# Performance work log

Measured on AMD Instinct MI355X. Metric: run time of the kernel, lower is better.

Reference implementation:

```python
import jax, jax.numpy as jnp
import numpy as np

TEMP = 0.05
EPS = 1e-8  # F.cosine_similarity eps

def setup_inputs() -> dict:
    key = jax.random.key(0)
    k1, k2 = jax.random.split(key)
    cls = jax.random.normal(k1, (4096, 1024), dtype=jnp.float32)
    hidden = jax.random.normal(k2, (4096, 1024), dtype=jnp.float32)
    return {"cls": cls, "hidden": hidden}

def _normalize(x):
    # matches F.cosine_similarity: divide by max(||x||, eps)
    n = jnp.sqrt(jnp.sum(x * x, axis=-1, keepdims=True))
    return x / jnp.maximum(n, EPS)

def reference(cls, hidden):
    a = _normalize(cls)          # [B, H]
    b = _normalize(hidden)       # [B, H]
    sim = jnp.einsum('ih,jh->ij', a, b) / TEMP  # [B, B] cosine sims / temp
    # cross-entropy with labels = arange(B): mean(logsumexp(row) - diag)
    lse = jax.nn.logsumexp(sim, axis=-1)        # [B]
    diag = jnp.diagonal(sim)                    # [B]
    return jnp.mean(lse - diag)
```

## Files before the change

### kernel.cpp

```cpp
#include <hip/hip_runtime.h>
#include <hip/hip_bf16.h>

typedef __attribute__((ext_vector_type(8))) short bf16x8;
typedef __attribute__((ext_vector_type(4))) float f32x4;

#define B_ROWS 4096
#define H_DIM  1024
#define TEMP_INV 20.0f
#define BM 256
#define BK 64
#define NT (H_DIM / BK)
#define NBN (B_ROWS / BM)

__device__ __forceinline__ void gload_lds16(const void* g, void* l) {
  __builtin_amdgcn_global_load_lds(
      (const __attribute__((address_space(1))) void*)g,
      (__attribute__((address_space(3))) void*)l, 16, 0, 0);
}

__global__ __launch_bounds__(256) void normalize_kernel(
    const float* __restrict__ cls, const float* __restrict__ hid,
    __hip_bfloat16* __restrict__ Abf, __hip_bfloat16* __restrict__ Bbf)
{
  const int w = threadIdx.x >> 6, lane = threadIdx.x & 63;
  const int r = blockIdx.x * 4 + w;
  const int rr = r & (B_ROWS - 1);
  const float* src = ((r < B_ROWS) ? cls : hid) + (size_t)rr * H_DIM;
  __hip_bfloat16* dst = ((r < B_ROWS) ? Abf : Bbf) + (size_t)rr * H_DIM;

  float4 v[4];
  float ss = 0.f;
  #pragma unroll
  for (int j = 0; j < 4; j++) {
    v[j] = reinterpret_cast<const float4*>(src)[j * 64 + lane];
    ss += v[j].x * v[j].x + v[j].y * v[j].y + v[j].z * v[j].z + v[j].w * v[j].w;
  }
  #pragma unroll
  for (int off = 1; off < 64; off <<= 1) ss += __shfl_xor(ss, off, 64);
  const float scale = 1.0f / fmaxf(sqrtf(ss), 1e-8f);

  #pragma unroll
  for (int j = 0; j < 4; j++) {
    union { ushort4 u; __hip_bfloat16 h[4]; } o;
    o.h[0] = __float2bfloat16(v[j].x * scale);
    o.h[1] = __float2bfloat16(v[j].y * scale);
    o.h[2] = __float2bfloat16(v[j].z * scale);
    o.h[3] = __float2bfloat16(v[j].w * scale);
    reinterpret_cast<ushort4*>(dst)[j * 64 + lane] = o.u;
  }
}


#define LDS_RD_A(BUF, MB)                                                     \
  { _Pragma("unroll") for (int mi = 0; mi < 4; mi++) {                        \
      _Pragma("unroll") for (int ks = 0; ks < 2; ks++) {                      \
        af[mi][ks] = *(const bf16x8*)(&As[BUF][(rA2 ^ (ks << 6)) + ((MB) + mi) * 2048]); } } }

#define LDS_RD_B(BUF, NB)                                                     \
  { _Pragma("unroll") for (int ni = 0; ni < 2; ni++) {                        \
      _Pragma("unroll") for (int ks = 0; ks < 2; ks++) {                      \
        bfr[(NB) + ni][ks] = *(const bf16x8*)(&Bs[BUF][(rB2 ^ (ks << 6)) + ((NB) + ni) * 2048]); } } }

#define MFMA16(MB, NB)                                                        \
  { __builtin_amdgcn_s_setprio(1);                                            \
    _Pragma("unroll") for (int mi = 0; mi < 4; mi++) {                        \
      _Pragma("unroll") for (int ni = 0; ni < 2; ni++) {                      \
        _Pragma("unroll") for (int ks = 0; ks < 2; ks++) {                    \
          acc[(MB) + mi][(NB) + ni] = __builtin_amdgcn_mfma_f32_16x16x32_bf16(\
              af[mi][ks], bfr[(NB) + ni][ks], acc[(MB) + mi][(NB) + ni], 0, 0, 0); } } } \
    __builtin_amdgcn_s_setprio(0); }

#define BARB() __builtin_amdgcn_s_barrier()

#define STAGE_A(BUF, TT, C)                                                   \
  gload_lds16(Abase + (size_t)(row0 + (C) * 64 + srow) * 2048 + (TT) * 128 + scolb, \
              &As[BUF][(C) * 8192 + tid * 16])
#define STAGE_B(BUF, TT, C)                                                   \
  gload_lds16(Bbase + (size_t)(col0 + (C) * 64 + srow) * 2048 + (TT) * 128 + scolb, \
              &Bs[BUF][(C) * 8192 + tid * 16])

#define KTILE(BUF, T_)                                                        \
  { const int Tn = (T_) + 1;                                                  \
    LDS_RD_A(BUF, 0);                                                         \
    if (Tn < NT) { STAGE_B(BUF ^ 1, Tn, 2); STAGE_B(BUF ^ 1, Tn, 3); }        \
    BARB(); MFMA16(0, 0); BARB();                                             \
    LDS_RD_B(BUF, 2);                                                         \
    if ((T_) + 2 < NT) { STAGE_A(BUF, (T_) + 2, 0); STAGE_A(BUF, (T_) + 2, 2); } \
    BARB(); MFMA16(0, 2); BARB();                                             \
    LDS_RD_A(BUF, 4);                                                         \
    if ((T_) + 2 < NT) { STAGE_B(BUF, (T_) + 2, 0); STAGE_B(BUF, (T_) + 2, 1); } \
    BARB(); MFMA16(4, 0); BARB();                                             \
    if ((T_) + 2 < NT) {                                                      \
      STAGE_A(BUF, (T_) + 2, 1); STAGE_A(BUF, (T_) + 2, 3);                   \
      asm volatile("s_waitcnt vmcnt(6)" ::: "memory");                        \
    } else if (Tn < NT) {                                                     \
      asm volatile("s_waitcnt vmcnt(0)" ::: "memory");                        \
    }                                                                         \
    BARB();                                                                   \
    if (Tn < NT) { LDS_RD_B(BUF ^ 1, 0); }                                    \
    MFMA16(4, 2); BARB(); }

__global__ __launch_bounds__(512, 2) void gemm_kernel(
    const __hip_bfloat16* __restrict__ A, const __hip_bfloat16* __restrict__ Bm,
    float* __restrict__ pp, float* __restrict__ diag)
{
  __shared__ __align__(16) char As[2][32768];
  __shared__ __align__(16) char Bs[2][32768];

  const int tid  = threadIdx.x;
  const int lane = tid & 63;
  const int w    = tid >> 6;
  const int wm   = w >> 2, wn = w & 3;

  const int fid = blockIdx.y * NBN + blockIdx.x;
  const int swz = (fid & 7) * 32 + (fid >> 3);
  const int bm = swz >> 4, bn = swz & 15;

  const long row0 = (long)bm * BM, col0 = (long)bn * BM;
  const char* Abase = (const char*)A;
  const char* Bbase = (const char*)Bm;

  const int srow  = tid >> 3;
  const int scolb = ((tid & 7) ^ ((tid >> 3) & 7)) << 4;

  const int dsw = (lane & 7) << 4;
  const int rA2 = (((wm * 128 + (lane & 15)) * 128) + ((lane >> 4) * 16)) ^ dsw;
  const int rB2 = (((wn * 64  + (lane & 15)) * 128) + ((lane >> 4) * 16)) ^ dsw;

  f32x4 acc[8][4] = {};
  bf16x8 af[4][2], bfr[4][2];

  #pragma unroll
  for (int c = 0; c < 4; c++) STAGE_A(0, 0, c);
  #pragma unroll
  for (int c = 0; c < 4; c++) STAGE_B(0, 0, c);
  STAGE_A(1, 1, 0); STAGE_A(1, 1, 2);
  STAGE_B(1, 1, 0); STAGE_B(1, 1, 1);
  STAGE_A(1, 1, 1); STAGE_A(1, 1, 3);
  asm volatile("s_waitcnt vmcnt(6)" ::: "memory");
  BARB();
  LDS_RD_B(0, 0);

  #pragma unroll 1
  for (int T = 0; T < NT; T += 2) {
    KTILE(0, T);
    KTILE(1, T + 1);
  }

  const bool isdiag = (bm == bn);
  const int g = lane >> 4;
  __syncthreads();
  float* lds_p = (float*)&As[0][0];

  #pragma unroll
  for (int m = 0; m < 8; m++) {
    const int rowb = (int)row0 + wm * 128 + m * 16 + g * 4;
    float p[4] = {0.f, 0.f, 0.f, 0.f};
    #pragma unroll
    for (int n = 0; n < 4; n++) {
      const int colb = (int)col0 + wn * 64 + n * 16 + (lane & 15);
      #pragma unroll
      for (int r = 0; r < 4; r++) {
        float sim = acc[m][n][r] * TEMP_INV;
        if (isdiag && (rowb + r == colb)) diag[rowb + r] = sim;
        p[r] += __expf(sim);
      }
    }
    #pragma unroll
    for (int r = 0; r < 4; r++) {
      float s = p[r];
      s += __shfl_xor(s, 1, 64);
      s += __shfl_xor(s, 2, 64);
      s += __shfl_xor(s, 4, 64);
      s += __shfl_xor(s, 8, 64);
      if ((lane & 15) == 0)
        lds_p[wn * 256 + wm * 128 + m * 16 + g * 4 + r] = s;
    }
  }
  __syncthreads();
  if (tid < 256) {
    float s = lds_p[tid] + lds_p[256 + tid] + lds_p[512 + tid] + lds_p[768 + tid];
    pp[(size_t)bn * B_ROWS + row0 + tid] = s;
  }
}

__global__ __launch_bounds__(1024) void finalize_kernel(
    const float* __restrict__ pp, const float* __restrict__ diag,
    float* __restrict__ out)
{
  int tid = threadIdx.x;
  float acc = 0.f;
  for (int i = tid; i < B_ROWS; i += 1024) {
    float s = 0.f;
    #pragma unroll
    for (int j = 0; j < NBN; j++) s += pp[(size_t)j * B_ROWS + i];
    acc += logf(s) - diag[i];
  }
  #pragma unroll
  for (int off = 1; off < 64; off <<= 1) acc += __shfl_xor(acc, off, 64);
  __shared__ float wsum[16];
  if ((tid & 63) == 0) wsum[tid >> 6] = acc;
  __syncthreads();
  if (tid == 0) {
    float t = 0.f;
    #pragma unroll
    for (int i = 0; i < 16; i++) t += wsum[i];
    out[0] = t * (1.0f / B_ROWS);
  }
}

extern "C" void kernel_launch(void* const* d_in, const int* in_sizes, int n_in,
                              void* d_out, int out_size, void* d_ws, size_t ws_size,
                              hipStream_t stream)
{
  const float* cls = (const float*)d_in[0];
  const float* hid = (const float*)d_in[1];
  float* out = (float*)d_out;
  char* ws = (char*)d_ws;

  __hip_bfloat16* Abf = (__hip_bfloat16*)ws;
  __hip_bfloat16* Bbf = (__hip_bfloat16*)(ws + (size_t)B_ROWS * H_DIM * 2);
  float* pp   = (float*)(ws + (size_t)B_ROWS * H_DIM * 4);
  float* diag = pp + (size_t)NBN * B_ROWS;

  hipLaunchKernelGGL(normalize_kernel, dim3(2 * B_ROWS / 4), dim3(256), 0, stream,
                     cls, hid, Abf, Bbf);
  hipLaunchKernelGGL(gemm_kernel, dim3(B_ROWS / BM, B_ROWS / BM), dim3(512), 0, stream,
                     Abf, Bbf, pp, diag);
  hipLaunchKernelGGL(finalize_kernel, dim3(1), dim3(1024), 0, stream,
                     pp, diag, out);
}
```

Baseline: 119.1 us.

## Restructure GEMM to 256x128 tiles, BK=32, triple-buffered LDS pipeline

Changes the fused cosine-sim GEMM from 256x256 tiles with 8 waves and a hand-interleaved double-buffered BK=64 schedule to 256x128 tiles with 4 waves, BK=32 and a three-stage LDS ring. Each iteration issues loads two tiles ahead, then reads fragments and runs 32 MFMAs. This aims for more blocks (512), a simpler schedule and deeper prefetch, with less LDS per block. The cost is less data reuse per block, more barriers and K iterations, and twice as many partial-sum rows for the finalize kernel. The finalize kernel loops over NBN, which is now 32.

```diff
diff --git a/kernel.cpp b/kernel.cpp
--- a/kernel.cpp
+++ b/kernel.cpp
@@ -8,9 +8,11 @@
 #define H_DIM  1024
 #define TEMP_INV 20.0f
 #define BM 256
-#define BK 64
+#define BN 128
+#define BK 32
 #define NT (H_DIM / BK)
-#define NBN (B_ROWS / BM)
+#define NBM (B_ROWS / BM)
+#define NBN (B_ROWS / BN)
 
 __device__ __forceinline__ void gload_lds16(const void* g, void* l) {
   __builtin_amdgcn_global_load_lds(
@@ -51,103 +53,88 @@
 }
 
 
-#define LDS_RD_A(BUF, MB)                                                     \
-  { _Pragma("unroll") for (int mi = 0; mi < 4; mi++) {                        \
-      _Pragma("unroll") for (int ks = 0; ks < 2; ks++) {                      \
-        af[mi][ks] = *(const bf16x8*)(&As[BUF][(rA2 ^ (ks << 6)) + ((MB) + mi) * 2048]); } } }
-
-#define LDS_RD_B(BUF, NB)                                                     \
-  { _Pragma("unroll") for (int ni = 0; ni < 2; ni++) {                        \
-      _Pragma("unroll") for (int ks = 0; ks < 2; ks++) {                      \
-        bfr[(NB) + ni][ks] = *(const bf16x8*)(&Bs[BUF][(rB2 ^ (ks << 6)) + ((NB) + ni) * 2048]); } } }
-
-#define MFMA16(MB, NB)                                                        \
+#define STAGE_A(BUF, TT, C)                                                   \
+  gload_lds16(Abase + (size_t)(row0 + (C) * 64 + srow) * 2048 + (TT) * 64 + scolb, \
+              &As[BUF][(C) * 4096 + tid * 16])
+#define STAGE_B(BUF, TT, C)                                                   \
+  gload_lds16(Bbase + (size_t)(col0 + (C) * 64 + srow) * 2048 + (TT) * 64 + scolb, \
+              &Bs[BUF][(C) * 4096 + tid * 16])
+
+#define STAGE6(BUF, TT)                                                       \
+  { STAGE_A(BUF, TT, 0); STAGE_A(BUF, TT, 1); STAGE_A(BUF, TT, 2);            \
+    STAGE_A(BUF, TT, 3); STAGE_B(BUF, TT, 0); STAGE_B(BUF, TT, 1); }
+
+#define RDFRAGS(BC)                                                           \
+  { _Pragma("unroll") for (int mi = 0; mi < 8; mi++)                          \
+      af[mi] = *(const bf16x8*)(&As[BC][rA + mi * 1024]);                     \
+    _Pragma("unroll") for (int ni = 0; ni < 4; ni++)                          \
+      bfr[ni] = *(const bf16x8*)(&Bs[BC][rB + ni * 1024]); }
+
+#define MFMA32()                                                              \
   { __builtin_amdgcn_s_setprio(1);                                            \
-    _Pragma("unroll") for (int mi = 0; mi < 4; mi++) {                        \
-      _Pragma("unroll") for (int ni = 0; ni < 2; ni++) {                      \
-        _Pragma("unroll") for (int ks = 0; ks < 2; ks++) {                    \
-          acc[(MB) + mi][(NB) + ni] = __builtin_amdgcn_mfma_f32_16x16x32_bf16(\
-              af[mi][ks], bfr[(NB) + ni][ks], acc[(MB) + mi][(NB) + ni], 0, 0, 0); } } } \
+    _Pragma("unroll") for (int mi = 0; mi < 8; mi++) {                        \
+      _Pragma("unroll") for (int ni = 0; ni < 4; ni++) {                      \
+        acc[mi][ni] = __builtin_amdgcn_mfma_f32_16x16x32_bf16(                \
+            af[mi], bfr[ni], acc[mi][ni], 0, 0, 0); } }                       \
     __builtin_amdgcn_s_setprio(0); }
 
 #define BARB() __builtin_amdgcn_s_barrier()
 
-#define STAGE_A(BUF, TT, C)                                                   \
-  gload_lds16(Abase + (size_t)(row0 + (C) * 64 + srow) * 2048 + (TT) * 128 + scolb, \
-              &As[BUF][(C) * 8192 + tid * 16])
-#define STAGE_B(BUF, TT, C)                                                   \
-  gload_lds16(Bbase + (size_t)(col0 + (C) * 64 + srow) * 2048 + (TT) * 128 + scolb, \
-              &Bs[BUF][(C) * 8192 + tid * 16])
-
-#define KTILE(BUF, T_)                                                        \
-  { const int Tn = (T_) + 1;                                                  \
-    LDS_RD_A(BUF, 0);                                                         \
-    if (Tn < NT) { STAGE_B(BUF ^ 1, Tn, 2); STAGE_B(BUF ^ 1, Tn, 3); }        \
-    BARB(); MFMA16(0, 0); BARB();                                             \
-    LDS_RD_B(BUF, 2);                                                         \
-    if ((T_) + 2 < NT) { STAGE_A(BUF, (T_) + 2, 0); STAGE_A(BUF, (T_) + 2, 2); } \
-    BARB(); MFMA16(0, 2); BARB();                                             \
-    LDS_RD_A(BUF, 4);                                                         \
-    if ((T_) + 2 < NT) { STAGE_B(BUF, (T_) + 2, 0); STAGE_B(BUF, (T_) + 2, 1); } \
-    BARB(); MFMA16(4, 0); BARB();                                             \
-    if ((T_) + 2 < NT) {                                                      \
-      STAGE_A(BUF, (T_) + 2, 1); STAGE_A(BUF, (T_) + 2, 3);                   \
-      asm volatile("s_waitcnt vmcnt(6)" ::: "memory");                        \
-    } else if (Tn < NT) {                                                     \
-      asm volatile("s_waitcnt vmcnt(0)" ::: "memory");                        \
-    }                                                                         \
-    BARB();                                                                   \
-    if (Tn < NT) { LDS_RD_B(BUF ^ 1, 0); }                                    \
-    MFMA16(4, 2); BARB(); }
-
-__global__ __launch_bounds__(512, 2) void gemm_kernel(
+#define ITER_F(BC, BN_, T_)                                                   \
+  { STAGE6(BN_, (T_) + 2); RDFRAGS(BC); MFMA32();                             \
+    asm volatile("s_waitcnt vmcnt(6)" ::: "memory"); BARB(); }
+#define ITER_W0(BC)                                                           \
+  { RDFRAGS(BC); MFMA32();                                                    \
+    asm volatile("s_waitcnt vmcnt(0)" ::: "memory"); BARB(); }
+#define ITER_L(BC)                                                            \
+  { RDFRAGS(BC); MFMA32(); }
+
+__global__ __launch_bounds__(256, 2) void gemm_kernel(
     const __hip_bfloat16* __restrict__ A, const __hip_bfloat16* __restrict__ Bm,
     float* __restrict__ pp, float* __restrict__ diag)
 {
-  __shared__ __align__(16) char As[2][32768];
-  __shared__ __align__(16) char Bs[2][32768];
+  __shared__ __align__(16) char As[3][16384];
+  __shared__ __align__(16) char Bs[3][8192];
 
   const int tid  = threadIdx.x;
   const int lane = tid & 63;
   const int w    = tid >> 6;
-  const int wm   = w >> 2, wn = w & 3;
+  const int wm   = w >> 1, wn = w & 1;
 
   const int fid = blockIdx.y * NBN + blockIdx.x;
-  const int swz = (fid & 7) * 32 + (fid >> 3);
-  const int bm = swz >> 4, bn = swz & 15;
-
-  const long row0 = (long)bm * BM, col0 = (long)bn * BM;
+  const int swz = (fid & 7) * 64 + (fid >> 3);
+  const int bm = swz >> 5, bn = swz & 31;
+
+  const long row0 = (long)bm * BM, col0 = (long)bn * BN;
   const char* Abase = (const char*)A;
   const char* Bbase = (const char*)Bm;
 
-  const int srow  = tid >> 3;
-  const int scolb = ((tid & 7) ^ ((tid >> 3) & 7)) << 4;
-
-  const int dsw = (lane & 7) << 4;
-  const int rA2 = (((wm * 128 + (lane & 15)) * 128) + ((lane >> 4) * 16)) ^ dsw;
-  const int rB2 = (((wn * 64  + (lane & 15)) * 128) + ((lane >> 4) * 16)) ^ dsw;
+  const int srow  = tid >> 2;
+  const int scolb = (((tid & 3) ^ ((tid >> 3) & 3)) << 4);
+
+  const int fr  = lane & 15;
+  const int xsl = ((lane >> 4) * 16) ^ ((fr & 6) << 3);
+  const int rA  = (wm * 128 + fr) * 64 + xsl;
+  const int rB  = (wn * 64  + fr) * 64 + xsl;
 
   f32x4 acc[8][4] = {};
-  bf16x8 af[4][2], bfr[4][2];
-
-  #pragma unroll
-  for (int c = 0; c < 4; c++) STAGE_A(0, 0, c);
-  #pragma unroll
-  for (int c = 0; c < 4; c++) STAGE_B(0, 0, c);
-  STAGE_A(1, 1, 0); STAGE_A(1, 1, 2);
-  STAGE_B(1, 1, 0); STAGE_B(1, 1, 1);
-  STAGE_A(1, 1, 1); STAGE_A(1, 1, 3);
+  bf16x8 af[8], bfr[4];
+
+  STAGE6(0, 0);
+  STAGE6(1, 1);
   asm volatile("s_waitcnt vmcnt(6)" ::: "memory");
   BARB();
-  LDS_RD_B(0, 0);
 
   #pragma unroll 1
-  for (int T = 0; T < NT; T += 2) {
-    KTILE(0, T);
-    KTILE(1, T + 1);
-  }
-
-  const bool isdiag = (bm == bn);
+  for (int T = 0; T < 30; T += 3) {
+    ITER_F(0, 2, T);
+    ITER_F(1, 0, T + 1);
+    ITER_F(2, 1, T + 2);
+  }
+  ITER_W0(0);
+  ITER_L(1);
+
+  const bool isdiag = ((bn >> 1) == bm);
   const int g = lane >> 4;
   __syncthreads();
   float* lds_p = (float*)&As[0][0];
@@ -158,7 +145,7 @@
     float p[4] = {0.f, 0.f, 0.f, 0.f};
     #pragma unroll
     for (int n = 0; n < 4; n++) {
-      const int colb = (int)col0 + wn * 64 + n * 16 + (lane & 15);
+      const int colb = (int)col0 + wn * 64 + n * 16 + fr;
       #pragma unroll
       for (int r = 0; r < 4; r++) {
         float sim = acc[m][n][r] * TEMP_INV;
@@ -173,13 +160,13 @@
       s += __shfl_xor(s, 2, 64);
       s += __shfl_xor(s, 4, 64);
       s += __shfl_xor(s, 8, 64);
-      if ((lane & 15) == 0)
+      if (fr == 0)
         lds_p[wn * 256 + wm * 128 + m * 16 + g * 4 + r] = s;
     }
   }
   __syncthreads();
-  if (tid < 256) {
-    float s = lds_p[tid] + lds_p[256 + tid] + lds_p[512 + tid] + lds_p[768 + tid];
+  {
+    float s = lds_p[tid] + lds_p[256 + tid];
     pp[(size_t)bn * B_ROWS + row0 + tid] = s;
   }
 }
@@ -225,7 +212,7 @@
 
   hipLaunchKernelGGL(normalize_kernel, dim3(2 * B_ROWS / 4), dim3(256), 0, stream,
                      cls, hid, Abf, Bbf);
-  hipLaunchKernelGGL(gemm_kernel, dim3(B_ROWS / BM, B_ROWS / BM), dim3(512), 0, stream,
+  hipLaunchKernelGGL(gemm_kernel, dim3(NBN, NBM), dim3(256), 0, stream,
                      Abf, Bbf, pp, diag);
   hipLaunchKernelGGL(finalize_kernel, dim3(1), dim3(1024), 0, stream,
                      pp, diag, out);
```

Measured after the change: 124.4 us. +4.5%, slower.
